# Kernel tuning notes

Hardware: AMD Instinct MI355X
Metric: run time of the kernel (lower is better)

The kernel has to match this reference:

```python
import jax, jax.numpy as jnp
import numpy as np

B, T, D, H, FF_MULT, WINDOW = 4, 2048, 256, 8, 4, 64
HD = D // H
FF = FF_MULT * D
EPS = 1e-5


def _layer_norm(x, g, b):
    m = jnp.mean(x, axis=-1, keepdims=True)
    v = jnp.mean(jnp.square(x - m), axis=-1, keepdims=True)
    return (x - m) / jnp.sqrt(v + EPS) * g + b


def setup_inputs() -> dict:
    key = jax.random.key(0)
    ks = jax.random.split(key, 6)
    scale = 0.02
    return {
        "x": jax.random.normal(ks[0], (B, T, D), jnp.float32),
        "ln1_g": jnp.ones((D,), jnp.float32),
        "ln1_b": jnp.zeros((D,), jnp.float32),
        "in_proj_w": jax.random.normal(ks[1], (D, 3 * D), jnp.float32) * scale,
        "in_proj_b": jnp.zeros((3 * D,), jnp.float32),
        "out_w": jax.random.normal(ks[2], (D, D), jnp.float32) * scale,
        "out_b": jnp.zeros((D,), jnp.float32),
        "ln2_g": jnp.ones((D,), jnp.float32),
        "ln2_b": jnp.zeros((D,), jnp.float32),
        "w1": jax.random.normal(ks[3], (D, FF), jnp.float32) * scale,
        "b1": jnp.zeros((FF,), jnp.float32),
        "w2": jax.random.normal(ks[4], (FF, D), jnp.float32) * scale,
        "b2": jnp.zeros((D,), jnp.float32),
        "window": WINDOW,
    }


def reference(x, ln1_g, ln1_b, in_proj_w, in_proj_b, out_w, out_b,
              ln2_g, ln2_b, w1, b1, w2, b2, window):
    Bv, Tv, Dv = x.shape
    xn = _layer_norm(x, ln1_g, ln1_b)                      # norm1(x) used as q,k,v
    qkv = xn @ in_proj_w + in_proj_b                       # [B,T,3D]
    q, k, v = jnp.split(qkv, 3, axis=-1)

    def to_heads(t):
        return t.reshape(Bv, Tv, H, HD).transpose(0, 2, 1, 3)  # [B,H,T,HD]

    q, k, v = to_heads(q), to_heads(k), to_heads(v)
    scores = jnp.einsum('bhqd,bhkd->bhqk', q, k) / jnp.sqrt(jnp.float32(HD))
    i = jnp.arange(Tv)[:, None]
    j = jnp.arange(Tv)[None, :]
    band = jnp.abs(j - i) <= window                        # True = allowed
    scores = jnp.where(band, scores, -jnp.inf)
    attn = jax.nn.softmax(scores, axis=-1)
    o = jnp.einsum('bhqk,bhkd->bhqd', attn, v)
    o = o.transpose(0, 2, 1, 3).reshape(Bv, Tv, Dv)
    h_out = o @ out_w + out_b                              # attn output
    y = x + h_out
    ff = _layer_norm(y, ln2_g, ln2_b)
    ff = jax.nn.gelu(ff @ w1 + b1, approximate=False) @ w2 + b2
    return x + ff                                          # note: residual from x, not y
```

## Files before the change

kernel.cpp:

```cpp
#include <hip/hip_runtime.h>
#include <math.h>

#define T_SEQ 2048

typedef float  fx4 __attribute__((ext_vector_type(4)));
typedef short  sx4 __attribute__((ext_vector_type(4)));
typedef short  sx8 __attribute__((ext_vector_type(8)));
typedef unsigned short u16;

static __device__ __forceinline__ u16 f2b(float f) {
  unsigned u = __builtin_bit_cast(unsigned, f);
  u += 0x7fffu + ((u >> 16) & 1u);
  return (u16)(u >> 16);
}
static __device__ __forceinline__ float b2f(u16 v) {
  unsigned u = ((unsigned)v) << 16;
  return __builtin_bit_cast(float, u);
}

static __device__ __forceinline__ fx4 mfma16(sx4 a, sx4 b, fx4 c) {
  return __builtin_amdgcn_mfma_f32_16x16x16bf16_1k(a, b, c, 0, 0, 0);
}
static __device__ __forceinline__ fx4 mfma32(sx8 a, sx8 b, fx4 c) {
  return __builtin_amdgcn_mfma_f32_16x16x32_bf16(a, b, c, 0, 0, 0);
}

static __device__ __forceinline__ void gload16(const void* g, void* l) {
  __builtin_amdgcn_global_load_lds(
      (const __attribute__((address_space(1))) unsigned*)g,
      (__attribute__((address_space(3))) unsigned*)l, 16, 0, 0);
}

__global__ __launch_bounds__(256) void prep_k(
    const float* __restrict__ x, const float* __restrict__ g1,
    const float* __restrict__ b1, u16* __restrict__ xn, u16* __restrict__ xb,
    const float* __restrict__ ipw, const float* __restrict__ outw,
    const float* __restrict__ w1, const float* __restrict__ w2,
    u16* __restrict__ ipwT, u16* __restrict__ outwT,
    u16* __restrict__ w1T, u16* __restrict__ w2T) {
  const int bid = blockIdx.x;
  if (bid < 2048) {
    const int row = bid * 4 + (threadIdx.x >> 6);
    const int l = threadIdx.x & 63;
    fx4 v = *(const fx4*)&x[(size_t)row * 256 + l * 4];
    float s = v.x + v.y + v.z + v.w;
    float q = v.x * v.x + v.y * v.y + v.z * v.z + v.w * v.w;
#pragma unroll
    for (int off = 1; off < 64; off <<= 1) {
      s += __shfl_xor(s, off);
      q += __shfl_xor(q, off);
    }
    const float mean = s * (1.0f / 256.0f);
    const float var = q * (1.0f / 256.0f) - mean * mean;
    const float rstd = rsqrtf(var + 1e-5f);
    fx4 gv = *(const fx4*)&g1[l * 4];
    fx4 bv = *(const fx4*)&b1[l * 4];
    sx4 o, xo;
    o[0] = (short)f2b((v.x - mean) * rstd * gv.x + bv.x);
    o[1] = (short)f2b((v.y - mean) * rstd * gv.y + bv.y);
    o[2] = (short)f2b((v.z - mean) * rstd * gv.z + bv.z);
    o[3] = (short)f2b((v.w - mean) * rstd * gv.w + bv.w);
    xo[0] = (short)f2b(v.x);
    xo[1] = (short)f2b(v.y);
    xo[2] = (short)f2b(v.z);
    xo[3] = (short)f2b(v.w);
    *(sx4*)&xn[(size_t)row * 256 + l * 4] = o;
    *(sx4*)&xb[(size_t)row * 256 + l * 4] = xo;
    return;
  }
  const int tb = bid - 2048;
  const float* in; u16* out; int K, N, loc;
  if (tb < 192)      { in = ipw;  out = ipwT;  K = 256;  N = 768;  loc = tb; }
  else if (tb < 256) { in = outw; out = outwT; K = 256;  N = 256;  loc = tb - 192; }
  else if (tb < 512) { in = w1;   out = w1T;   K = 256;  N = 1024; loc = tb - 256; }
  else               { in = w2;   out = w2T;   K = 1024; N = 256;  loc = tb - 512; }
  const int ntx = N >> 5;
  const int by = (loc / ntx) << 5;
  const int bx = (loc % ntx) << 5;
  __shared__ float t[32][33];
  const int c = threadIdx.x & 31, r0 = threadIdx.x >> 5;
#pragma unroll
  for (int i = 0; i < 4; ++i)
    t[r0 + i * 8][c] = in[(size_t)(by + r0 + i * 8) * N + bx + c];
  __syncthreads();
#pragma unroll
  for (int i = 0; i < 4; ++i) {
    const int r = r0 + i * 8;
    out[(size_t)(bx + r) * K + by + c] = f2b(t[c][r]);
  }
}

template <int BM, int BN, int KD, int ND, int OP, int NGRP>
__global__ __launch_bounds__(512) void gemm6_k(const u16* __restrict__ A,
                                               const u16* __restrict__ Wt,
                                               const float* __restrict__ bias,
                                               const float* __restrict__ resid,
                                               void* __restrict__ outp) {
  constexpr int BK = 64;
  constexpr int NTH = 512;
  constexpr int WTM = BM / 2, WTN = BN / 4;
  constexpr int FM = WTM / 16, FN = WTN / 16;
  constexpr int NT = KD / BK;
  __shared__ __align__(16) char smem[(2 * BM + 2 * BN) * BK * 2];
  auto As = (u16(*)[BM][BK])smem;
  auto Bs = (u16(*)[BN][BK])(smem + 2 * BM * BK * 2);
  const int tid = threadIdx.x;
  const int id = blockIdx.x;
  const int bm = ((id & 7) + 8 * ((id >> 3) / NGRP)) * BM;
  const int bn = ((id >> 3) % NGRP) * BN;
  const int l = tid & 63, wid = tid >> 6;
  const int wr = wid >> 2, wc = wid & 3;
  const int lq = l & 15, lg = l >> 4;

  auto stage = [&](int buf, int k0) {
#pragma unroll
    for (int i = 0; i < (BM * 8 + NTH - 1) / NTH; ++i) {
      const int p = tid + i * NTH;
      if (BM * 8 % NTH == 0 || p < BM * 8) {
        const int row = p >> 3, ch = p & 7;
        gload16(&A[(size_t)(bm + row) * KD + k0 + ((ch ^ (row & 7)) << 3)],
                &As[buf][row][ch << 3]);
      }
    }
#pragma unroll
    for (int i = 0; i < (BN * 8 + NTH - 1) / NTH; ++i) {
      const int p = tid + i * NTH;
      if (BN * 8 % NTH == 0 || p < BN * 8) {
        const int row = p >> 3, ch = p & 7;
        gload16(&Wt[(size_t)(bn + row) * KD + k0 + ((ch ^ (row & 7)) << 3)],
                &Bs[buf][row][ch << 3]);
      }
    }
  };

  fx4 acc[FM][FN] = {};
  stage(0, 0);
  int cur = 0;
  for (int t = 0; t < NT; ++t) {
    __syncthreads();
    if (t + 1 < NT) stage(cur ^ 1, (t + 1) * BK);
#pragma unroll
    for (int kk = 0; kk < BK; kk += 32) {
      sx8 aF[FM], bF[FN];
#pragma unroll
      for (int m = 0; m < FM; ++m) {
        const int row = wr * WTM + m * 16 + lq;
        aF[m] = *(const sx8*)&As[cur][row][((((kk >> 3) + lg) ^ (row & 7)) << 3)];
      }
#pragma unroll
      for (int n = 0; n < FN; ++n) {
        const int row = wc * WTN + n * 16 + lq;
        bF[n] = *(const sx8*)&Bs[cur][row][((((kk >> 3) + lg) ^ (row & 7)) << 3)];
      }
#pragma unroll
      for (int m = 0; m < FM; ++m)
#pragma unroll
        for (int n = 0; n < FN; ++n) acc[m][n] = mfma32(aF[m], bF[n], acc[m][n]);
    }
    cur ^= 1;
  }

  __syncthreads();
  if (OP == 1) {
    auto C = (float(*)[BN + 8])smem;
#pragma unroll
    for (int m = 0; m < FM; ++m)
#pragma unroll
      for (int n = 0; n < FN; ++n) {
        const int col = wc * WTN + n * 16 + lq;
        const float bv = bias[bn + col];
#pragma unroll
        for (int r = 0; r < 4; ++r)
          C[wr * WTM + m * 16 + lg * 4 + r][col] = acc[m][n][r] + bv;
      }
    __syncthreads();
    constexpr int CH = (BM * BN / 4) / NTH;
#pragma unroll
    for (int i = 0; i < CH; ++i) {
      const int t = tid + i * NTH;
      const int row = t / (BN / 4), c = t % (BN / 4);
      fx4 v = *(const fx4*)&C[row][c * 4];
      v += *(const fx4*)&resid[(size_t)(bm + row) * ND + bn + c * 4];
      *(fx4*)&((float*)outp)[(size_t)(bm + row) * ND + bn + c * 4] = v;
    }
  } else {
    auto C = (u16(*)[BN + 8])smem;
#pragma unroll
    for (int m = 0; m < FM; ++m)
#pragma unroll
      for (int n = 0; n < FN; ++n) {
        const int col = wc * WTN + n * 16 + lq;
        const float bv = bias[bn + col];
#pragma unroll
        for (int r = 0; r < 4; ++r) {
          float v = acc[m][n][r] + bv;
          if (OP == 2) v = 0.5f * v * (1.0f + erff(v * 0.70710678118654752f));
          C[wr * WTM + m * 16 + lg * 4 + r][col] = f2b(v);
        }
      }
    __syncthreads();
    constexpr int CH = (BM * BN / 8) / NTH;
#pragma unroll
    for (int i = 0; i < CH; ++i) {
      const int t = tid + i * NTH;
      const int row = t / (BN / 8), c = t % (BN / 8);
      *(sx8*)&((u16*)outp)[(size_t)(bm + row) * ND + bn + c * 8] = *(const sx8*)&C[row][c * 8];
    }
  }
}

__global__ __launch_bounds__(512) void gemmln_k(const u16* __restrict__ A,
                                                const u16* __restrict__ Wt,
                                                const float* __restrict__ bias,
                                                const u16* __restrict__ xb,
                                                const float* __restrict__ g,
                                                const float* __restrict__ bv2,
                                                u16* __restrict__ yn) {
  __shared__ __align__(16) char smem[70656];
  auto As = (u16(*)[16][64])smem;
  auto Bs = (u16(*)[256][64])(smem + 4096);
  auto red = (float(*)[8][2])(smem + 69632);
  auto Ys = (u16(*)[264])smem;
  const int tid = threadIdx.x;
  const int bm = blockIdx.x * 16;
  const int l = tid & 63, wc = tid >> 6;
  const int lq = l & 15, lg = l >> 4;

  auto stage = [&](int buf, int k0) {
    if (tid < 128) {
      const int row = tid >> 3, ch = tid & 7;
      gload16(&A[(size_t)(bm + row) * 256 + k0 + ((ch ^ (row & 7)) << 3)],
              &As[buf][row][ch << 3]);
    }
#pragma unroll
    for (int i = 0; i < 4; ++i) {
      const int p = tid + i * 512;
      const int row = p >> 3, ch = p & 7;
      gload16(&Wt[(size_t)row * 256 + k0 + ((ch ^ (row & 7)) << 3)],
              &Bs[buf][row][ch << 3]);
    }
  };

  fx4 acc[2] = {};
  stage(0, 0);
  int cur = 0;
  for (int t = 0; t < 4; ++t) {
    __syncthreads();
    if (t + 1 < 4) stage(cur ^ 1, (t + 1) * 64);
#pragma unroll
    for (int kk = 0; kk < 64; kk += 32) {
      const sx8 aF = *(const sx8*)&As[cur][lq][((((kk >> 3) + lg) ^ (lq & 7)) << 3)];
#pragma unroll
      for (int n = 0; n < 2; ++n) {
        const int brow = wc * 32 + n * 16 + lq;
        const sx8 bF = *(const sx8*)&Bs[cur][brow][((((kk >> 3) + lg) ^ (brow & 7)) << 3)];
        acc[n] = mfma32(aF, bF, acc[n]);
      }
    }
    cur ^= 1;
  }

  float vv[2][4];
  float s[4] = {}, q[4] = {};
#pragma unroll
  for (int n = 0; n < 2; ++n) {
    const int col = wc * 32 + n * 16 + lq;
    const float bb = bias[col];
#pragma unroll
    for (int r = 0; r < 4; ++r) {
      const int row = bm + lg * 4 + r;
      const float v = acc[n][r] + bb + b2f(xb[(size_t)row * 256 + col]);
      vv[n][r] = v;
      s[r] += v;
      q[r] += v * v;
    }
  }
#pragma unroll
  for (int off = 1; off < 16; off <<= 1) {
#pragma unroll
    for (int r = 0; r < 4; ++r) {
      s[r] += __shfl_xor(s[r], off);
      q[r] += __shfl_xor(q[r], off);
    }
  }
  __syncthreads();
  if (lq == 0) {
#pragma unroll
    for (int r = 0; r < 4; ++r) {
      red[lg * 4 + r][wc][0] = s[r];
      red[lg * 4 + r][wc][1] = q[r];
    }
  }
  __syncthreads();
  float mean4[4], rs4[4];
#pragma unroll
  for (int r = 0; r < 4; ++r) {
    const int rr = lg * 4 + r;
    float st = 0.f, qt = 0.f;
#pragma unroll
    for (int w8 = 0; w8 < 8; ++w8) {
      st += red[rr][w8][0];
      qt += red[rr][w8][1];
    }
    mean4[r] = st * (1.0f / 256.0f);
    const float var = qt * (1.0f / 256.0f) - mean4[r] * mean4[r];
    rs4[r] = rsqrtf(var + 1e-5f);
  }
  __syncthreads();
#pragma unroll
  for (int n = 0; n < 2; ++n) {
    const int col = wc * 32 + n * 16 + lq;
    const float gc = g[col], bc = bv2[col];
#pragma unroll
    for (int r = 0; r < 4; ++r)
      Ys[lg * 4 + r][col] = f2b((vv[n][r] - mean4[r]) * rs4[r] * gc + bc);
  }
  __syncthreads();
  {
    const int row = tid >> 5, c = tid & 31;
    *(sx8*)&yn[(size_t)(bm + row) * 256 + c * 8] = *(const sx8*)&Ys[row][c * 8];
  }
}

__global__ __launch_bounds__(512) void attn_k(const u16* __restrict__ qkv,
                                              u16* __restrict__ o) {
  __shared__ u16 Qs[128][32];
  __shared__ u16 Ks[256][32];
  __shared__ u16 Vs[32][264];
  const int blk = blockIdx.x;
  const int tile = blk & 15;
  const int bh = blk >> 4;
  const int h = bh & 7;
  const int b = bh >> 3;
  const int q0 = tile << 7;
  const int kstart = max(0, q0 - 64);
  const int kend = min(T_SEQ, q0 + 192);
  const int nk = kend - kstart;
  const int tid = threadIdx.x;
  const float scale = 0.17677669529663687f;

  {
    const int r = tid >> 2, c8 = (tid & 3) << 3;
    gload16(&qkv[(size_t)(b * T_SEQ + q0 + r) * 768 + h * 32 + c8], &Qs[r][c8]);
  }
  for (int r0 = 0; r0 < nk; r0 += 128) {
    const int r = r0 + (tid >> 2);
    if (r < nk) {
      const int c8 = (tid & 3) << 3;
      gload16(&qkv[(size_t)(b * T_SEQ + kstart + r) * 768 + 256 + h * 32 + c8], &Ks[r][c8]);
    }
  }
  for (int e = tid * 4; e < nk * 32; e += 2048) {
    const int r = e >> 5, c = e & 31;
    sx4 v = *(const sx4*)&qkv[(size_t)(b * T_SEQ + kstart + r) * 768 + 512 + h * 32 + c];
    Vs[c + 0][r] = v[0];
    Vs[c + 1][r] = v[1];
    Vs[c + 2][r] = v[2];
    Vs[c + 3][r] = v[3];
  }
  __syncthreads();

  const int w = tid >> 6, l = tid & 63;
  const int lq = l & 15, lg = l >> 4;
  const int qw0 = q0 + w * 16;
  const int iq = qw0 + lq;
  const sx8 qB = *(const sx8*)&Qs[w * 16 + lq][8 * lg];
  float lsum = 0.0f;
  fx4 acc0 = {0.f, 0.f, 0.f, 0.f}, acc1 = {0.f, 0.f, 0.f, 0.f};
  const int rt0 = max(0, qw0 - 64 - kstart) >> 4;
  const int rt1 = (min(kend, qw0 + 80) - kstart) >> 4;
  for (int rt = rt0; rt < rt1; ++rt) {
    const int kb = kstart + (rt << 4);
    const sx8 kA = *(const sx8*)&Ks[(rt << 4) + lq][8 * lg];
    fx4 zero = {0.f, 0.f, 0.f, 0.f};
    fx4 sc = mfma32(kA, qB, zero);
    sx4 pB;
#pragma unroll
    for (int r = 0; r < 4; ++r) {
      const int dd = kb + 4 * lg + r - iq;
      const float sv = (dd >= -64 && dd <= 64) ? fminf(sc[r] * scale, 30.0f) : -100.0f;
      const float p = __expf(sv);
      lsum += p;
      pB[r] = (short)f2b(p);
    }
    const sx4 vA0 = *(const sx4*)&Vs[lq][(rt << 4) + 4 * lg];
    const sx4 vA1 = *(const sx4*)&Vs[16 + lq][(rt << 4) + 4 * lg];
    acc0 = mfma16(vA0, pB, acc0);
    acc1 = mfma16(vA1, pB, acc1);
  }
  lsum += __shfl_xor(lsum, 16);
  lsum += __shfl_xor(lsum, 32);
  const float rl = 1.0f / lsum;

  __syncthreads();
  auto Os = (u16(*)[32])Qs;
#pragma unroll
  for (int r = 0; r < 4; ++r) {
    Os[w * 16 + lq][4 * lg + r] = f2b(acc0[r] * rl);
    Os[w * 16 + lq][16 + 4 * lg + r] = f2b(acc1[r] * rl);
  }
  __syncthreads();
  {
    const int row = tid >> 2, c = tid & 3;
    *(sx8*)&o[(size_t)(b * T_SEQ + q0 + row) * 256 + h * 32 + c * 8] =
        *(const sx8*)&Os[row][c * 8];
  }
}

extern "C" void kernel_launch(void* const* d_in, const int* in_sizes, int n_in,
                              void* d_out, int out_size, void* d_ws, size_t ws_size,
                              hipStream_t stream) {
  const float* x    = (const float*)d_in[0];
  const float* ln1g = (const float*)d_in[1];
  const float* ln1b = (const float*)d_in[2];
  const float* ipw  = (const float*)d_in[3];
  const float* ipb  = (const float*)d_in[4];
  const float* outw = (const float*)d_in[5];
  const float* outb = (const float*)d_in[6];
  const float* ln2g = (const float*)d_in[7];
  const float* ln2b = (const float*)d_in[8];
  const float* w1   = (const float*)d_in[9];
  const float* b1   = (const float*)d_in[10];
  const float* w2   = (const float*)d_in[11];
  const float* b2   = (const float*)d_in[12];

  char* ws = (char*)d_ws;
  u16*   xn   = (u16*)(ws);
  u16*   qkvb = (u16*)(ws + (4ull << 20));
  u16*   o    = (u16*)(ws + (16ull << 20));
  u16*   yn   = (u16*)(ws + (20ull << 20));
  u16*   hh   = (u16*)(ws + (24ull << 20));
  u16*   xb   = (u16*)(ws + (40ull << 20));
  u16*   ipwT = (u16*)(ws + (44ull << 20));
  u16*   outwT= (u16*)(ws + (44ull << 20) + (512ull << 10));
  u16*   w1T  = (u16*)(ws + (45ull << 20));
  u16*   w2T  = (u16*)(ws + (45ull << 20) + (512ull << 10));

  prep_k<<<2816, 256, 0, stream>>>(x, ln1g, ln1b, xn, xb, ipw, outw, w1, w2,
                                   ipwT, outwT, w1T, w2T);
  gemm6_k<64, 128, 256, 768, 0, 6><<<768, 512, 0, stream>>>(xn, ipwT, ipb, nullptr, qkvb);
  attn_k<<<512, 512, 0, stream>>>(qkvb, o);
  gemmln_k<<<512, 512, 0, stream>>>(o, outwT, outb, xb, ln2g, ln2b, yn);
  gemm6_k<128, 128, 256, 1024, 2, 8><<<512, 512, 0, stream>>>(yn, w1T, b1, nullptr, hh);
  gemm6_k<32, 128, 1024, 256, 1, 2><<<512, 512, 0, stream>>>(hh, w2T, b2, x, (float*)d_out);
}
```

Measured before the change: 59.25 us.

## Write QKV in head-major layout and move weight transposes into attention launch

The QKV GEMM epilogue now scatters its output into separate head-major Q, K and V buffers, so each attention block reads contiguous per-head rows instead of strided slices of the 768-wide QKV rows. The transposes of the out-proj, w1 and w2 weights move from the prep kernel into extra blocks of the attention launch, which leaves prep with only LayerNorm and the in-proj transpose. This is meant to improve coalescing in attention loads and to overlap the weight conversion with attention work. The cost is a scattered epilogue store in the QKV GEMM and extra blocks sharing the attention grid.

Result: no change. 59.54 us (median of 2 runs) (+0.5%).

```diff
diff --git a/kernel.cpp b/kernel.cpp
--- a/kernel.cpp
+++ b/kernel.cpp
@@ -34,10 +34,7 @@
 __global__ __launch_bounds__(256) void prep_k(
     const float* __restrict__ x, const float* __restrict__ g1,
     const float* __restrict__ b1, u16* __restrict__ xn, u16* __restrict__ xb,
-    const float* __restrict__ ipw, const float* __restrict__ outw,
-    const float* __restrict__ w1, const float* __restrict__ w2,
-    u16* __restrict__ ipwT, u16* __restrict__ outwT,
-    u16* __restrict__ w1T, u16* __restrict__ w2T) {
+    const float* __restrict__ ipw, u16* __restrict__ ipwT) {
   const int bid = blockIdx.x;
   if (bid < 2048) {
     const int row = bid * 4 + (threadIdx.x >> 6);
@@ -68,25 +65,19 @@
     *(sx4*)&xb[(size_t)row * 256 + l * 4] = xo;
     return;
   }
-  const int tb = bid - 2048;
-  const float* in; u16* out; int K, N, loc;
-  if (tb < 192)      { in = ipw;  out = ipwT;  K = 256;  N = 768;  loc = tb; }
-  else if (tb < 256) { in = outw; out = outwT; K = 256;  N = 256;  loc = tb - 192; }
-  else if (tb < 512) { in = w1;   out = w1T;   K = 256;  N = 1024; loc = tb - 256; }
-  else               { in = w2;   out = w2T;   K = 1024; N = 256;  loc = tb - 512; }
-  const int ntx = N >> 5;
-  const int by = (loc / ntx) << 5;
-  const int bx = (loc % ntx) << 5;
+  const int loc = bid - 2048;
+  const int by = (loc / 24) << 5;
+  const int bx = (loc % 24) << 5;
   __shared__ float t[32][33];
   const int c = threadIdx.x & 31, r0 = threadIdx.x >> 5;
 #pragma unroll
   for (int i = 0; i < 4; ++i)
-    t[r0 + i * 8][c] = in[(size_t)(by + r0 + i * 8) * N + bx + c];
+    t[r0 + i * 8][c] = ipw[(size_t)(by + r0 + i * 8) * 768 + bx + c];
   __syncthreads();
 #pragma unroll
   for (int i = 0; i < 4; ++i) {
     const int r = r0 + i * 8;
-    out[(size_t)(bx + r) * K + by + c] = f2b(t[c][r]);
+    ipwT[(size_t)(bx + r) * 256 + by + c] = f2b(t[c][r]);
   }
 }
 
@@ -95,7 +86,10 @@
                                                const u16* __restrict__ Wt,
                                                const float* __restrict__ bias,
                                                const float* __restrict__ resid,
-                                               void* __restrict__ outp) {
+                                               void* __restrict__ outp,
+                                               u16* __restrict__ qh,
+                                               u16* __restrict__ kh,
+                                               u16* __restrict__ vh) {
   constexpr int BK = 64;
   constexpr int NTH = 512;
   constexpr int WTM = BM / 2, WTN = BN / 4;
@@ -204,7 +198,18 @@
     for (int i = 0; i < CH; ++i) {
       const int t = tid + i * NTH;
       const int row = t / (BN / 8), c = t % (BN / 8);
-      *(sx8*)&((u16*)outp)[(size_t)(bm + row) * ND + bn + c * 8] = *(const sx8*)&C[row][c * 8];
+      if (OP == 3) {
+        const int n = bn + c * 8;
+        const int sect = n >> 8, within = n & 255;
+        const int head = within >> 5, d = within & 31;
+        const int grow = bm + row;
+        const int b = grow >> 11, tt = grow & 2047;
+        u16* dst = sect == 0 ? qh : (sect == 1 ? kh : vh);
+        *(sx8*)&dst[(((size_t)(b * 8 + head) * 2048 + tt) << 5) + d] =
+            *(const sx8*)&C[row][c * 8];
+      } else {
+        *(sx8*)&((u16*)outp)[(size_t)(bm + row) * ND + bn + c * 8] = *(const sx8*)&C[row][c * 8];
+      }
     }
   }
 }
@@ -322,37 +327,69 @@
   }
 }
 
-__global__ __launch_bounds__(512) void attn_k(const u16* __restrict__ qkv,
-                                              u16* __restrict__ o) {
-  __shared__ u16 Qs[128][32];
-  __shared__ u16 Ks[256][32];
-  __shared__ u16 Vs[32][264];
+__global__ __launch_bounds__(512) void attn_k(const u16* __restrict__ qh,
+                                              const u16* __restrict__ kh,
+                                              const u16* __restrict__ vh,
+                                              u16* __restrict__ o,
+                                              const float* __restrict__ outw,
+                                              const float* __restrict__ w1,
+                                              const float* __restrict__ w2,
+                                              u16* __restrict__ outwT,
+                                              u16* __restrict__ w1T,
+                                              u16* __restrict__ w2T) {
+  __shared__ __align__(16) char smem[41728];
   const int blk = blockIdx.x;
+  const int tid = threadIdx.x;
+
+  if (blk >= 512) {
+    const int tb = blk - 512;
+    const float* in; u16* out; int K, N, loc;
+    if (tb < 64)       { in = outw; out = outwT; K = 256;  N = 256;  loc = tb; }
+    else if (tb < 320) { in = w1;   out = w1T;   K = 256;  N = 1024; loc = tb - 64; }
+    else               { in = w2;   out = w2T;   K = 1024; N = 256;  loc = tb - 320; }
+    const int ntx = N >> 5;
+    const int by = (loc / ntx) << 5;
+    const int bx = (loc % ntx) << 5;
+    auto t = (float(*)[33])smem;
+    const int c = tid & 31, r0 = tid >> 5;
+#pragma unroll
+    for (int i = 0; i < 2; ++i)
+      t[r0 + i * 16][c] = in[(size_t)(by + r0 + i * 16) * N + bx + c];
+    __syncthreads();
+#pragma unroll
+    for (int i = 0; i < 2; ++i) {
+      const int r = r0 + i * 16;
+      out[(size_t)(bx + r) * K + by + c] = f2b(t[c][r]);
+    }
+    return;
+  }
+
+  auto Qs = (u16(*)[32])smem;
+  auto Ks = (u16(*)[32])(smem + 8192);
+  auto Vs = (u16(*)[268])(smem + 24576);
   const int tile = blk & 15;
   const int bh = blk >> 4;
-  const int h = bh & 7;
-  const int b = bh >> 3;
   const int q0 = tile << 7;
   const int kstart = max(0, q0 - 64);
   const int kend = min(T_SEQ, q0 + 192);
   const int nk = kend - kstart;
-  const int tid = threadIdx.x;
   const float scale = 0.17677669529663687f;
+  const size_t hbase = (size_t)bh * T_SEQ;
 
   {
     const int r = tid >> 2, c8 = (tid & 3) << 3;
-    gload16(&qkv[(size_t)(b * T_SEQ + q0 + r) * 768 + h * 32 + c8], &Qs[r][c8]);
+    gload16(&qh[((hbase + q0 + r) << 5) + c8], &Qs[r][c8]);
   }
   for (int r0 = 0; r0 < nk; r0 += 128) {
     const int r = r0 + (tid >> 2);
     if (r < nk) {
       const int c8 = (tid & 3) << 3;
-      gload16(&qkv[(size_t)(b * T_SEQ + kstart + r) * 768 + 256 + h * 32 + c8], &Ks[r][c8]);
+      gload16(&kh[((hbase + kstart + r) << 5) + c8], &Ks[r][c8]);
     }
   }
   for (int e = tid * 4; e < nk * 32; e += 2048) {
     const int r = e >> 5, c = e & 31;
-    sx4 v = *(const sx4*)&qkv[(size_t)(b * T_SEQ + kstart + r) * 768 + 512 + h * 32 + c];
+    sx4 v = *(const sx4*)&vh[((hbase + kstart + r) << 5) + c];
     Vs[c + 0][r] = v[0];
     Vs[c + 1][r] = v[1];
     Vs[c + 2][r] = v[2];
@@ -401,6 +438,7 @@
   }
   __syncthreads();
   {
+    const int b = bh >> 3, h = bh & 7;
     const int row = tid >> 2, c = tid & 3;
     *(sx8*)&o[(size_t)(b * T_SEQ + q0 + row) * 256 + h * 32 + c * 8] =
         *(const sx8*)&Os[row][c * 8];
@@ -426,7 +464,9 @@
 
   char* ws = (char*)d_ws;
   u16*   xn   = (u16*)(ws);
-  u16*   qkvb = (u16*)(ws + (4ull << 20));
+  u16*   qh   = (u16*)(ws + (4ull << 20));
+  u16*   kh   = (u16*)(ws + (8ull << 20));
+  u16*   vh   = (u16*)(ws + (12ull << 20));
   u16*   o    = (u16*)(ws + (16ull << 20));
   u16*   yn   = (u16*)(ws + (20ull << 20));
   u16*   hh   = (u16*)(ws + (24ull << 20));
@@ -436,11 +476,13 @@
   u16*   w1T  = (u16*)(ws + (45ull << 20));
   u16*   w2T  = (u16*)(ws + (45ull << 20) + (512ull << 10));
 
-  prep_k<<<2816, 256, 0, stream>>>(x, ln1g, ln1b, xn, xb, ipw, outw, w1, w2,
-                                   ipwT, outwT, w1T, w2T);
-  gemm6_k<64, 128, 256, 768, 0, 6><<<768, 512, 0, stream>>>(xn, ipwT, ipb, nullptr, qkvb);
-  attn_k<<<512, 512, 0, stream>>>(qkvb, o);
+  prep_k<<<2240, 256, 0, stream>>>(x, ln1g, ln1b, xn, xb, ipw, ipwT);
+  gemm6_k<64, 128, 256, 768, 3, 6><<<768, 512, 0, stream>>>(
+      xn, ipwT, ipb, nullptr, nullptr, qh, kh, vh);
+  attn_k<<<1088, 512, 0, stream>>>(qh, kh, vh, o, outw, w1, w2, outwT, w1T, w2T);
   gemmln_k<<<512, 512, 0, stream>>>(o, outwT, outb, xb, ln2g, ln2b, yn);
-  gemm6_k<128, 128, 256, 1024, 2, 8><<<512, 512, 0, stream>>>(yn, w1T, b1, nullptr, hh);
-  gemm6_k<32, 128, 1024, 256, 1, 2><<<512, 512, 0, stream>>>(hh, w2T, b2, x, (float*)d_out);
-}
+  gemm6_k<128, 128, 256, 1024, 2, 8><<<512, 512, 0, stream>>>(
+      yn, w1T, b1, nullptr, hh, nullptr, nullptr, nullptr);
+  gemm6_k<32, 128, 1024, 256, 1, 2><<<512, 512, 0, stream>>>(
+      hh, w2T, b2, x, (float*)d_out, nullptr, nullptr, nullptr);
+}
```
